# Optimization experiments

Measured on AMD Instinct MI355X. Metric: run time of the kernel, lower is better.

Reference implementation:

```python
import jax, jax.numpy as jnp
import numpy as np

B, I, O, G = 4096, 256, 256, 8
GRID_MIN, GRID_MAX, RHO = -2.0, 2.0, 1.0


def setup_inputs() -> dict:
    key = jax.random.key(0)
    ks = jax.random.split(key, 8)
    return {
        "x_re": jax.random.normal(ks[0], (B, I), dtype=jnp.float32),
        "x_im": jax.random.normal(ks[1], (B, I), dtype=jnp.float32),
        "realweights": jax.random.normal(ks[2], (I, O, G, G), dtype=jnp.float32),
        "complexweights": jax.random.normal(ks[3], (I, O, G, G), dtype=jnp.float32),
        "silu_weight_re": jax.random.normal(ks[4], (I, O), dtype=jnp.float32),
        "silu_weight_im": jax.random.normal(ks[5], (I, O), dtype=jnp.float32),
        "silu_bias_re": 0.1 * jax.random.normal(ks[6], (I, O), dtype=jnp.float32),
        "silu_bias_im": 0.1 * jax.random.normal(ks[7], (I, O), dtype=jnp.float32),
    }


def reference(x_re, x_im, realweights, complexweights,
              silu_weight_re, silu_weight_im, silu_bias_re, silu_bias_im):
    # Complex grid: grid[u, v] = lin[u] + i * lin[v]
    lin = jnp.linspace(GRID_MIN, GRID_MAX, G, dtype=x_re.dtype)
    # |x - grid|^2 = (x_re - lin_u)^2 + (x_im - lin_v)^2  -> (B, I, G, G)
    dre = x_re[:, :, None, None] - lin[None, None, :, None]
    dim = x_im[:, :, None, None] - lin[None, None, None, :]
    basis = jnp.exp(-(dre * dre + dim * dim) / RHO)  # real-valued (B, I, G, G)
    # RBF contraction: real and imaginary output channels
    out_re = jnp.einsum('biuv,iouv->bo', basis, realweights)
    out_im = jnp.einsum('biuv,iouv->bo', basis, complexweights)
    # Complex SiLU (complex_weight variant): silu applied component-wise,
    # then complex-multiplied by silu_weight, plus bias, summed over i.
    s_re = jax.nn.silu(x_re)  # (B, I)
    s_im = jax.nn.silu(x_im)
    out_re = out_re + s_re @ silu_weight_re - s_im @ silu_weight_im + jnp.sum(silu_bias_re, axis=0)
    out_im = out_im + s_im @ silu_weight_re + s_re @ silu_weight_im + jnp.sum(silu_bias_im, axis=0)
    # Return complex output as stacked (real, imag): (B, O, 2)
    return jnp.stack([out_re, out_im], axis=-1)
```

## Files before the change

kernel.cpp:

```cpp
#include <hip/hip_runtime.h>
#include <stdint.h>

typedef float floatx4 __attribute__((ext_vector_type(4)));
typedef short short8 __attribute__((ext_vector_type(8)));

constexpr int I_SZ = 256, O_SZ = 256, NCOL = 512, B_SZ = 4096;
constexpr int KSTEPS = 264;
constexpr int SPC = 33;
constexpr float GSTEP = 4.0f / 7.0f;
constexpr float NLOG2E = -1.44269504088896f;

__device__ __forceinline__ uint32_t pk_bf16(float lo, float hi) {
  return __builtin_amdgcn_perm(__float_as_uint(hi), __float_as_uint(lo), 0x07060302u);
}
__device__ __forceinline__ short rne_bf16(float f) {
  uint32_t u = __float_as_uint(f);
  return (short)((u + 0x7FFFu + ((u >> 16) & 1u)) >> 16);
}

__device__ __forceinline__ void gload_lds16(const void* g, void* l) {
  __builtin_amdgcn_global_load_lds((const __attribute__((address_space(1))) void*)g,
                                   (__attribute__((address_space(3))) void*)l,
                                   16, 0, 0);
}

__device__ __forceinline__ float silu_f(float a) {
  return a * __builtin_amdgcn_rcpf(1.f + __builtin_amdgcn_exp2f(a * NLOG2E));
}

__global__ void pack_weights(const float* __restrict__ rw, const float* __restrict__ cw,
                             const float* __restrict__ swre, const float* __restrict__ swim,
                             short* __restrict__ wpack) {
  int idx = blockIdx.x * 256 + threadIdx.x;
  int kb = idx >> 12;
  int rem = idx & 4095;
  int n = rem >> 3, gp = rem & 7;
  int g = gp ^ (n & 7);
  int o = n >> 1, c = n & 1;
  float w[8];
  if (kb < 256) {
    const float* W = (c ? cw : rw) + (((size_t)kb * O_SZ + o) << 6) + (g << 3);
    float4 a = *(const float4*)W;
    float4 b = *(const float4*)(W + 4);
    w[0] = a.x; w[1] = a.y; w[2] = a.z; w[3] = a.w;
    w[4] = b.x; w[5] = b.y; w[6] = b.z; w[7] = b.w;
  } else {
    int kp0 = ((kb - 256) << 6) + (g << 3);
    #pragma unroll
    for (int e = 0; e < 8; ++e) {
      int kp = kp0 + e, i = kp >> 1, ci = kp & 1;
      float a = swre[i * O_SZ + o], b = swim[i * O_SZ + o];
      w[e] = (c == 0) ? (ci == 0 ? a : -b) : (ci == 0 ? b : a);
    }
  }
  uint32_t h[8];
  #pragma unroll
  for (int e = 0; e < 8; ++e) h[e] = (uint32_t)(uint16_t)rne_bf16(w[e]);
  uint4 val = make_uint4(h[0] | (h[1] << 16), h[2] | (h[3] << 16),
                         h[4] | (h[5] << 16), h[6] | (h[7] << 16));
  *(uint4*)(wpack + (size_t)idx * 8) = val;
}

__global__ void bias_sums(const float* __restrict__ bre, const float* __restrict__ bim,
                          float* __restrict__ bsum) {
  int n = blockIdx.x, o = n >> 1, l = threadIdx.x;
  const float* src = ((n & 1) ? bim : bre) + o;
  float s = 0.f;
  #pragma unroll
  for (int a = 0; a < 4; ++a) s += src[(size_t)(a * 64 + l) * O_SZ];
  #pragma unroll
  for (int off = 32; off; off >>= 1) s += __shfl_down(s, off, 64);
  if (l == 0) bsum[n] = s;
}

__global__ __launch_bounds__(256, 4) void cvkan_gemm(
    const float* __restrict__ xre, const float* __restrict__ xim,
    const short* __restrict__ wpack, const float* __restrict__ bsum,
    float* __restrict__ out) {
  __shared__ __align__(16) short Bs[128 * 64];
  __shared__ __align__(16) short As[128 * 64];

  const int tid = threadIdx.x;
  const int bid = blockIdx.x;
  const int kch = bid & 7;
  const int mn = bid >> 3;
  const int mt = mn >> 2, nt = mn & 3;
  const int b0 = mt * 128, n0 = nt * 128;
  const int l = tid & 63, w = tid >> 6;
  const int wr = w >> 1, wc = w & 1;
  const int lm = l & 15, q = l >> 4;
  const int r = tid >> 1, h = tid & 1;

  floatx4 acc[4][4] = {};

  for (int s = kch * SPC; s < (kch + 1) * SPC; ++s) {
    {
      const short* src = wpack + (((size_t)s * NCOL + n0) << 6) + (tid << 3);
      short* ldst = Bs + (w << 9);
      gload_lds16(src,        ldst);
      gload_lds16(src + 2048, ldst + 2048);
      gload_lds16(src + 4096, ldst + 4096);
      gload_lds16(src + 6144, ldst + 6144);
    }

    if (s < 256) {
      float xr = xre[(size_t)(b0 + r) * I_SZ + s];
      float xi = xim[(size_t)(b0 + r) * I_SZ + s];
      float eiv[8];
      #pragma unroll
      for (int v = 0; v < 8; ++v) {
        float d = xi - (-2.0f + v * GSTEP);
        eiv[v] = __builtin_amdgcn_exp2f(d * d * NLOG2E);
      }
      #pragma unroll
      for (int uu = 0; uu < 4; ++uu) {
        int u = h * 4 + uu;
        float d = xr - (-2.0f + u * GSTEP);
        float er = __builtin_amdgcn_exp2f(d * d * NLOG2E);
        uint4 val = make_uint4(pk_bf16(er * eiv[0], er * eiv[1]),
                               pk_bf16(er * eiv[2], er * eiv[3]),
                               pk_bf16(er * eiv[4], er * eiv[5]),
                               pk_bf16(er * eiv[6], er * eiv[7]));
        *(uint4*)(As + (r << 6) + ((u ^ (r & 7)) << 3)) = val;
      }
    } else {
      int sl = s - 256;
      #pragma unroll
      for (int gg = 0; gg < 4; ++gg) {
        int g = h * 4 + gg;
        const float* pr = xre + (size_t)(b0 + r) * I_SZ + (sl << 5) + (g << 2);
        const float* pi = xim + (size_t)(b0 + r) * I_SZ + (sl << 5) + (g << 2);
        uint4 val = make_uint4(pk_bf16(silu_f(pr[0]), silu_f(pi[0])),
                               pk_bf16(silu_f(pr[1]), silu_f(pi[1])),
                               pk_bf16(silu_f(pr[2]), silu_f(pi[2])),
                               pk_bf16(silu_f(pr[3]), silu_f(pi[3])));
        *(uint4*)(As + (r << 6) + ((g ^ (r & 7)) << 3)) = val;
      }
    }

    __builtin_amdgcn_s_waitcnt(0);
    __syncthreads();

    short8 bf[4][2];
    #pragma unroll
    for (int nn = 0; nn < 4; ++nn) {
      int col = wc * 64 + nn * 16 + lm;
      const short* bp = Bs + (col << 6);
      bf[nn][0] = *(const short8*)(bp + ((q       ^ (col & 7)) << 3));
      bf[nn][1] = *(const short8*)(bp + (((q + 4) ^ (col & 7)) << 3));
    }
    #pragma unroll
    for (int mm = 0; mm < 4; ++mm) {
      int row = wr * 64 + mm * 16 + lm;
      const short* ap = As + (row << 6);
      short8 a0 = *(const short8*)(ap + ((q       ^ (row & 7)) << 3));
      short8 a1 = *(const short8*)(ap + (((q + 4) ^ (row & 7)) << 3));
      #pragma unroll
      for (int nn = 0; nn < 4; ++nn) {
        acc[mm][nn] = __builtin_amdgcn_mfma_f32_16x16x32_bf16(a0, bf[nn][0], acc[mm][nn], 0, 0, 0);
        acc[mm][nn] = __builtin_amdgcn_mfma_f32_16x16x32_bf16(a1, bf[nn][1], acc[mm][nn], 0, 0, 0);
      }
    }
    __syncthreads();
  }

  #pragma unroll
  for (int nn = 0; nn < 4; ++nn) {
    int col = n0 + wc * 64 + nn * 16 + lm;
    float bv = (kch == 7) ? bsum[col] : 0.0f;
    #pragma unroll
    for (int mm = 0; mm < 4; ++mm) {
      int row0 = b0 + wr * 64 + mm * 16 + (q << 2);
      #pragma unroll
      for (int r2 = 0; r2 < 4; ++r2)
        atomicAdd(out + (size_t)(row0 + r2) * NCOL + col, acc[mm][nn][r2] + bv);
    }
  }
}

extern "C" void kernel_launch(void* const* d_in, const int* in_sizes, int n_in,
                              void* d_out, int out_size, void* d_ws, size_t ws_size,
                              hipStream_t stream) {
  const float* xre  = (const float*)d_in[0];
  const float* xim  = (const float*)d_in[1];
  const float* rw   = (const float*)d_in[2];
  const float* cw   = (const float*)d_in[3];
  const float* swre = (const float*)d_in[4];
  const float* swim = (const float*)d_in[5];
  const float* bre  = (const float*)d_in[6];
  const float* bim  = (const float*)d_in[7];
  float* out = (float*)d_out;

  short* wpack = (short*)d_ws;
  float* bsum  = (float*)((char*)d_ws + (size_t)KSTEPS * NCOL * 64 * 2);

  hipMemsetAsync(d_out, 0, (size_t)B_SZ * NCOL * sizeof(float), stream);
  pack_weights<<<(KSTEPS * NCOL * 8) / 256, 256, 0, stream>>>(rw, cw, swre, swim, wpack);
  bias_sums<<<NCOL, 64, 0, stream>>>(bre, bim, bsum);
  cvkan_gemm<<<1024, 256, 0, stream>>>(xre, xim, wpack, bsum, out);
}
```

Before: 223.6 us.

## Pre-transpose x to fp16 and rebalance K-chunks so each does one SiLU step

Adds a transpose kernel that writes x_re/x_im as fp16 in [I][B] layout, so the GEMM's per-step x loads become coalesced across rows instead of strided by I. It also reassigns K steps so each of the 8 chunks handles 32 RBF steps plus exactly one SiLU step, which balances the work across chunks. The x loads are issued before the weight prefetch. Storing x in fp16 before the exp computation adds rounding error, and the extra transpose kernel adds launch and memory-traffic cost.

```diff
diff --git a/kernel.cpp b/kernel.cpp
--- a/kernel.cpp
+++ b/kernel.cpp
@@ -1,4 +1,5 @@
 #include <hip/hip_runtime.h>
+#include <hip/hip_fp16.h>
 #include <stdint.h>
 
 typedef float floatx4 __attribute__((ext_vector_type(4)));
@@ -6,7 +7,6 @@
 
 constexpr int I_SZ = 256, O_SZ = 256, NCOL = 512, B_SZ = 4096;
 constexpr int KSTEPS = 264;
-constexpr int SPC = 33;
 constexpr float GSTEP = 4.0f / 7.0f;
 constexpr float NLOG2E = -1.44269504088896f;
 
@@ -61,6 +61,31 @@
   *(uint4*)(wpack + (size_t)idx * 8) = val;
 }
 
+__global__ void transpose_x(const float* __restrict__ xre, const float* __restrict__ xim,
+                            __half* __restrict__ xT) {
+  __shared__ float tile[64][65];
+  int bt = blockIdx.x & 63;
+  int it = (blockIdx.x >> 6) & 3;
+  int c  = blockIdx.x >> 8;
+  const float* src = (c ? xim : xre);
+  int b0 = bt << 6, i0 = it << 6;
+  int t = threadIdx.x;
+  int il = t & 63, bh = t >> 6;
+  #pragma unroll
+  for (int k = 0; k < 16; ++k) {
+    int bl = bh + (k << 2);
+    tile[bl][il] = src[(size_t)(b0 + bl) * I_SZ + i0 + il];
+  }
+  __syncthreads();
+  int bl2 = t & 63, ih = t >> 6;
+  __half* dst = xT + ((size_t)c * I_SZ + i0) * B_SZ + b0;
+  #pragma unroll
+  for (int k = 0; k < 16; ++k) {
+    int il2 = ih + (k << 2);
+    dst[(size_t)il2 * B_SZ + bl2] = __float2half(tile[bl2][il2]);
+  }
+}
+
 __global__ void bias_sums(const float* __restrict__ bre, const float* __restrict__ bim,
                           float* __restrict__ bsum) {
   int n = blockIdx.x, o = n >> 1, l = threadIdx.x;
@@ -75,6 +100,7 @@
 
 __global__ __launch_bounds__(256, 4) void cvkan_gemm(
     const float* __restrict__ xre, const float* __restrict__ xim,
+    const __half* __restrict__ xT,
     const short* __restrict__ wpack, const float* __restrict__ bsum,
     float* __restrict__ out) {
   __shared__ __align__(16) short Bs[128 * 64];
@@ -91,9 +117,20 @@
   const int lm = l & 15, q = l >> 4;
   const int r = tid >> 1, h = tid & 1;
 
+  const __half* xTre = xT;
+  const __half* xTim = xT + (size_t)I_SZ * B_SZ;
+
   floatx4 acc[4][4] = {};
 
-  for (int s = kch * SPC; s < (kch + 1) * SPC; ++s) {
+  for (int j = 0; j < 33; ++j) {
+    const int s = (j < 32) ? (kch * 32 + j) : (256 + kch);
+
+    float xr = 0.f, xi = 0.f;
+    if (j < 32) {
+      xr = __half2float(xTre[(size_t)s * B_SZ + b0 + r]);
+      xi = __half2float(xTim[(size_t)s * B_SZ + b0 + r]);
+    }
+
     {
       const short* src = wpack + (((size_t)s * NCOL + n0) << 6) + (tid << 3);
       short* ldst = Bs + (w << 9);
@@ -103,9 +140,7 @@
       gload_lds16(src + 6144, ldst + 6144);
     }
 
-    if (s < 256) {
-      float xr = xre[(size_t)(b0 + r) * I_SZ + s];
-      float xi = xim[(size_t)(b0 + r) * I_SZ + s];
+    if (j < 32) {
       float eiv[8];
       #pragma unroll
       for (int v = 0; v < 8; ++v) {
@@ -124,7 +159,7 @@
         *(uint4*)(As + (r << 6) + ((u ^ (r & 7)) << 3)) = val;
       }
     } else {
-      int sl = s - 256;
+      int sl = kch;
       #pragma unroll
       for (int gg = 0; gg < 4; ++gg) {
         int g = h * 4 + gg;
@@ -191,11 +226,14 @@
   const float* bim  = (const float*)d_in[7];
   float* out = (float*)d_out;
 
+  size_t wpack_bytes = (size_t)KSTEPS * NCOL * 64 * 2;
   short* wpack = (short*)d_ws;
-  float* bsum  = (float*)((char*)d_ws + (size_t)KSTEPS * NCOL * 64 * 2);
+  float* bsum  = (float*)((char*)d_ws + wpack_bytes);
+  __half* xT   = (__half*)((char*)d_ws + wpack_bytes + 2048);
 
   hipMemsetAsync(d_out, 0, (size_t)B_SZ * NCOL * sizeof(float), stream);
   pack_weights<<<(KSTEPS * NCOL * 8) / 256, 256, 0, stream>>>(rw, cw, swre, swim, wpack);
+  transpose_x<<<512, 256, 0, stream>>>(xre, xim, xT);
   bias_sums<<<NCOL, 64, 0, stream>>>(bre, bim, bsum);
-  cvkan_gemm<<<1024, 256, 0, stream>>>(xre, xim, wpack, bsum, out);
-}
+  cvkan_gemm<<<1024, 256, 0, stream>>>(xre, xim, xT, wpack, bsum, out);
+}
```

Result: faster. 205.9 us (-7.9%).
